# Kernel tuning notes

Hardware: AMD Instinct MI355X
Metric: run time of the kernel (lower is better)

The kernel has to match this reference:

```python
import jax, jax.numpy as jnp
import numpy as np

EMBED = 256
HID = EMBED * 4
NUM_EXPERTS = 4
WINDOW = 16
B, T = 4, 4096
EPS = 1e-5


def _ln(x, g, b):
    m = jnp.mean(x, axis=-1, keepdims=True)
    v = jnp.mean(jnp.square(x - m), axis=-1, keepdims=True)
    return (x - m) / jnp.sqrt(v + EPS) * g + b


def setup_inputs() -> dict:
    key = jax.random.key(0)
    ks = jax.random.split(key, 16)
    s = 0.02
    d = {
        'x': jax.random.normal(ks[0], (B, T, EMBED), jnp.float32),
        'ln1_g': jnp.ones((EMBED,), jnp.float32),
        'ln1_b': jnp.zeros((EMBED,), jnp.float32),
        'qkv_w': jax.random.normal(ks[1], (EMBED, 3 * EMBED), jnp.float32) * s,
        'qkv_b': jnp.zeros((3 * EMBED,), jnp.float32),
        'proj_w': jax.random.normal(ks[2], (EMBED, EMBED), jnp.float32) * s,
        'proj_b': jnp.zeros((EMBED,), jnp.float32),
        'attn_gate': jnp.ones((EMBED,), jnp.float32),
        'ln2_g': jnp.ones((EMBED,), jnp.float32),
        'ln2_b': jnp.zeros((EMBED,), jnp.float32),
        'gating_w': jax.random.normal(ks[3], (EMBED, NUM_EXPERTS), jnp.float32) * s,
        'gating_b': jnp.zeros((NUM_EXPERTS,), jnp.float32),
        'e_w1': jax.random.normal(ks[4], (NUM_EXPERTS, EMBED, HID), jnp.float32) * s,
        'e_b1': jnp.zeros((NUM_EXPERTS, HID), jnp.float32),
        'e_w2': jax.random.normal(ks[5], (NUM_EXPERTS, HID, EMBED), jnp.float32) * s,
        'e_b2': jnp.zeros((NUM_EXPERTS, EMBED), jnp.float32),
    }
    return d


def reference(x, ln1_g, ln1_b, qkv_w, qkv_b, proj_w, proj_b, attn_gate,
              ln2_g, ln2_b, gating_w, gating_b, e_w1, e_b1, e_w2, e_b2):
    Bx, Tx, C = x.shape
    # --- sparse attention branch ---
    h = _ln(x, ln1_g, ln1_b)
    qkv = h @ qkv_w + qkv_b                      # [B,T,3C]
    q, k, v = jnp.split(qkv, 3, axis=-1)
    scores = jnp.einsum('btc,bsc->bts', q, k) / jnp.sqrt(jnp.float32(C))
    idx = jnp.arange(Tx)
    diff = idx[:, None] - idx[None, :]           # i - j
    in_window = (diff >= 0) & (diff <= WINDOW)
    # faithful to torch code: scores outside the window (but causal) stay 0,
    # positions above the diagonal become -inf; softmax over full row
    scores = jnp.where(in_window, scores, 0.0)
    scores = jnp.where(diff >= 0, scores, -jnp.inf)
    att = jax.nn.softmax(scores, axis=-1)        # [B,T,T]
    a_out = jnp.einsum('bts,bsc->btc', att, v) * attn_gate
    x = x + a_out @ proj_w + proj_b
    # --- dense all-expert MoE branch ---
    h2 = _ln(x, ln2_g, ln2_b)
    gates = jax.nn.softmax(h2 @ gating_w + gating_b, axis=-1)     # [B,T,E]
    hid = jax.nn.gelu(jnp.einsum('btc,ech->bteh', h2, e_w1) + e_b1,
                      approximate=False)                           # [B,T,E,H]
    eo = jnp.einsum('bteh,eho->bteo', hid, e_w2) + e_b2            # [B,T,E,C]
    moe_out = jnp.einsum('bte,bteo->bto', gates, eo)
    return x + moe_out
```

## Files before the change

kernel.cpp:

```cpp
#include <hip/hip_runtime.h>
#include <hip/hip_bf16.h>
#include <math.h>

#define T_   4096
#define B_   4
#define C_   256
#define C3_  768
#define H_   1024
#define E_   4
#define M_   (B_*T_)
#define NCH_ 64
#define CHL_ (T_/NCH_)
#define KH_  4096

typedef __attribute__((ext_vector_type(8))) short short8;
typedef __attribute__((ext_vector_type(4))) float floatx4;

__device__ __forceinline__ float b2f(unsigned short u) {
  union { unsigned int i; float f; } x; x.i = ((unsigned int)u) << 16; return x.f;
}
__device__ __forceinline__ unsigned short f2b(float f) {
  __hip_bfloat16 h = __float2bfloat16(f);
  return *reinterpret_cast<unsigned short*>(&h);
}
__device__ __forceinline__ void unpack8(uint4 a, float* f) {
  unsigned int w[4] = {a.x, a.y, a.z, a.w};
  #pragma unroll
  for (int i = 0; i < 4; i++) {
    union { unsigned int u; float g; } lo, hi;
    lo.u = w[i] << 16; hi.u = w[i] & 0xffff0000u;
    f[2*i] = lo.g; f[2*i+1] = hi.g;
  }
}
__device__ __forceinline__ void gl_lds16(const void* g, void* l) {
  __builtin_amdgcn_global_load_lds(
      (const __attribute__((address_space(1))) void*)g,
      (__attribute__((address_space(3))) void*)l, 16, 0, 0);
}
__device__ __forceinline__ float gelu_s(float v) {
  float e = __expf(-1.702f * v);
  return v * __builtin_amdgcn_rcpf(1.0f + e);
}
__device__ __forceinline__ unsigned int pk_fp8x4(float a, float b, float c, float d) {
  unsigned int v = 0;
  v = __builtin_amdgcn_cvt_pk_fp8_f32(a, b, v, false);
  v = __builtin_amdgcn_cvt_pk_fp8_f32(c, d, v, true);
  return v;
}
__device__ __forceinline__ unsigned char f2fp8(float v) {
  return (unsigned char)(__builtin_amdgcn_cvt_pk_fp8_f32(v, v, 0, false) & 0xff);
}

__global__ __launch_bounds__(256) void transpose_cvt(
    const float* __restrict__ src, unsigned short* __restrict__ dst, int K, int N,
    int dstLd, size_t dstZStride) {
  __shared__ float tile[32][33];
  src += (size_t)blockIdx.z * K * N;
  dst += (size_t)blockIdx.z * dstZStride;
  int n0 = blockIdx.x * 32, k0 = blockIdx.y * 32;
  int tx = threadIdx.x, ty = threadIdx.y;
  #pragma unroll
  for (int i = 0; i < 32; i += 8)
    tile[ty + i][tx] = src[(size_t)(k0 + ty + i) * N + n0 + tx];
  __syncthreads();
  #pragma unroll
  for (int i = 0; i < 32; i += 8)
    dst[(size_t)(n0 + ty + i) * dstLd + k0 + tx] = f2b(tile[tx][ty + i]);
}

__global__ __launch_bounds__(256) void transpose_w2_fp8(
    const float* __restrict__ src, unsigned char* __restrict__ dst) {
  __shared__ float tile[32][33];
  int e = blockIdx.z;
  src += (size_t)e * H_ * C_;
  int h0 = blockIdx.x * 32, c0 = blockIdx.y * 32;
  int tx = threadIdx.x, ty = threadIdx.y;
  #pragma unroll
  for (int i = 0; i < 32; i += 8)
    tile[ty + i][tx] = src[(size_t)(h0 + ty + i) * C_ + c0 + tx];
  __syncthreads();
  int k = e * H_ + h0 + tx;
  int kp = (k & ~63) | ((k & 48) >> 2) | ((k & 12) << 2) | (k & 3);
  #pragma unroll
  for (int i = 0; i < 32; i += 8)
    dst[(size_t)(c0 + ty + i) * KH_ + kp] = f2fp8(tile[tx][ty + i] * 256.0f);
}

__global__ __launch_bounds__(256) void ln1_kernel(
    const float* __restrict__ x, const float* __restrict__ g,
    const float* __restrict__ b, unsigned short* __restrict__ h) {
  __shared__ float red[4];
  int row = blockIdx.x, tid = threadIdx.x;
  float v = x[(size_t)row * C_ + tid];
  float s = v;
  #pragma unroll
  for (int o = 32; o; o >>= 1) s += __shfl_xor(s, o);
  if ((tid & 63) == 0) red[tid >> 6] = s;
  __syncthreads();
  float mean = (red[0] + red[1] + red[2] + red[3]) * (1.0f / C_);
  __syncthreads();
  float d = v - mean;
  float q = d * d;
  #pragma unroll
  for (int o = 32; o; o >>= 1) q += __shfl_xor(q, o);
  if ((tid & 63) == 0) red[tid >> 6] = q;
  __syncthreads();
  float var = (red[0] + red[1] + red[2] + red[3]) * (1.0f / C_);
  h[(size_t)row * C_ + tid] = f2b(d * rsqrtf(var + 1e-5f) * g[tid] + b[tid]);
}

__global__ __launch_bounds__(256) void ln2_gates_kernel(
    const float* __restrict__ x1, const float* __restrict__ g,
    const float* __restrict__ b, const float* __restrict__ gw,
    const float* __restrict__ gb, unsigned short* __restrict__ h2,
    float* __restrict__ gates) {
  __shared__ float red[4];
  __shared__ float redg[4][4];
  int row = blockIdx.x, tid = threadIdx.x;
  float v = x1[(size_t)row * C_ + tid];
  float s = v;
  #pragma unroll
  for (int o = 32; o; o >>= 1) s += __shfl_xor(s, o);
  if ((tid & 63) == 0) red[tid >> 6] = s;
  __syncthreads();
  float mean = (red[0] + red[1] + red[2] + red[3]) * (1.0f / C_);
  __syncthreads();
  float d = v - mean;
  float q = d * d;
  #pragma unroll
  for (int o = 32; o; o >>= 1) q += __shfl_xor(q, o);
  if ((tid & 63) == 0) red[tid >> 6] = q;
  __syncthreads();
  float var = (red[0] + red[1] + red[2] + red[3]) * (1.0f / C_);
  float hv = d * rsqrtf(var + 1e-5f) * g[tid] + b[tid];
  h2[(size_t)row * C_ + tid] = f2b(hv);
  float p0 = hv * gw[tid * 4 + 0];
  float p1 = hv * gw[tid * 4 + 1];
  float p2 = hv * gw[tid * 4 + 2];
  float p3 = hv * gw[tid * 4 + 3];
  #pragma unroll
  for (int o = 32; o; o >>= 1) {
    p0 += __shfl_xor(p0, o); p1 += __shfl_xor(p1, o);
    p2 += __shfl_xor(p2, o); p3 += __shfl_xor(p3, o);
  }
  if ((tid & 63) == 0) {
    int w = tid >> 6;
    redg[w][0] = p0; redg[w][1] = p1; redg[w][2] = p2; redg[w][3] = p3;
  }
  __syncthreads();
  if (tid == 0) {
    float t4[4];
    #pragma unroll
    for (int e = 0; e < 4; e++)
      t4[e] = redg[0][e] + redg[1][e] + redg[2][e] + redg[3][e] + gb[e];
    float m = fmaxf(fmaxf(t4[0], t4[1]), fmaxf(t4[2], t4[3]));
    float zs = 0.f;
    #pragma unroll
    for (int e = 0; e < 4; e++) { t4[e] = __expf(t4[e] - m); zs += t4[e]; }
    float inv = 1.0f / zs;
    #pragma unroll
    for (int e = 0; e < 4; e++) gates[(size_t)row * 4 + e] = t4[e] * inv;
  }
}

__global__ __launch_bounds__(256) void scan1_kernel(const unsigned short* __restrict__ qkv,
                                                    float* __restrict__ S) {
  int b = blockIdx.x >> 6, ch = blockIdx.x & 63, c = threadIdx.x;
  float s = 0.f;
  size_t base = ((size_t)b * T_ + (size_t)ch * CHL_) * C3_ + 512 + c;
  for (int t = 0; t < CHL_; t++) s += b2f(qkv[base + (size_t)t * C3_]);
  S[((size_t)b * NCH_ + ch) * C_ + c] = s;
}
__global__ __launch_bounds__(256) void scan2_kernel(float* __restrict__ S) {
  int b = blockIdx.x, c = threadIdx.x;
  float run = 0.f;
  for (int ch = 0; ch < NCH_; ch++) {
    size_t i = ((size_t)b * NCH_ + ch) * C_ + c;
    float t = S[i]; S[i] = run; run += t;
  }
}
__global__ __launch_bounds__(256) void scan3_kernel(const unsigned short* __restrict__ qkv,
                                                    const float* __restrict__ S,
                                                    unsigned short* __restrict__ Pb) {
  int b = blockIdx.x >> 6, ch = blockIdx.x & 63, c = threadIdx.x;
  float run = S[((size_t)b * NCH_ + ch) * C_ + c];
  size_t row0 = (size_t)b * T_ + (size_t)ch * CHL_;
  for (int t = 0; t < CHL_; t++) {
    run += b2f(qkv[(row0 + t) * C3_ + 512 + c]);
    Pb[(row0 + t) * C_ + c] = f2b(run);
  }
}

__global__ __launch_bounds__(256) void attn_kernel(
    const unsigned short* __restrict__ qkv, const unsigned short* __restrict__ Pb,
    const float* __restrict__ gate, unsigned short* __restrict__ aout) {
  int wave = threadIdx.x >> 6, lane = threadIdx.x & 63;
  int r = blockIdx.x * 4 + wave;
  int t = r & (T_ - 1);
  int g = lane >> 4, u = lane & 15;
  const unsigned short* qp = qkv + (size_t)r * C3_ + (u << 4);
  float qv[16];
  unpack8(*(const uint4*)qp, qv);
  unpack8(*(const uint4*)(qp + 8), qv + 8);
  float sc[5];
  #pragma unroll
  for (int rnd = 0; rnd < 5; rnd++) {
    int j = rnd * 4 + g;
    int jj = t - 16 + j;
    bool valid = (j <= 16) && (jj >= 0);
    float d = 0.f;
    if (valid) {
      const unsigned short* kp = qkv + (size_t)(r - 16 + j) * C3_ + 256 + (u << 4);
      float kv[16];
      unpack8(*(const uint4*)kp, kv);
      unpack8(*(const uint4*)(kp + 8), kv + 8);
      #pragma unroll
      for (int c = 0; c < 16; c++) d += qv[c] * kv[c];
    }
    d += __shfl_xor(d, 1); d += __shfl_xor(d, 2);
    d += __shfl_xor(d, 4); d += __shfl_xor(d, 8);
    sc[rnd] = valid ? d * 0.0625f : -1e30f;
  }
  float m = fmaxf(fmaxf(fmaxf(sc[0], sc[1]), fmaxf(sc[2], sc[3])), sc[4]);
  m = fmaxf(m, __shfl_xor(m, 16));
  m = fmaxf(m, __shfl_xor(m, 32));
  if (t > 16) m = fmaxf(m, 0.0f);
  float ev[5], Zp = 0.f;
  #pragma unroll
  for (int rnd = 0; rnd < 5; rnd++) {
    ev[rnd] = (sc[rnd] > -1e29f) ? __expf(sc[rnd] - m) : 0.f;
    Zp += ev[rnd];
  }
  Zp += __shfl_xor(Zp, 16);
  Zp += __shfl_xor(Zp, 32);
  float e0v = 0.f;
  if (t > 16) { e0v = __expf(-m); Zp += e0v * (float)(t - 16); }
  float vp[16];
  #pragma unroll
  for (int c = 0; c < 16; c++) vp[c] = 0.f;
  #pragma unroll
  for (int rnd = 0; rnd < 5; rnd++) {
    if (ev[rnd] != 0.f) {
      int j = rnd * 4 + g;
      const unsigned short* vpp = qkv + (size_t)(r - 16 + j) * C3_ + 512 + (u << 4);
      float vv[16];
      unpack8(*(const uint4*)vpp, vv);
      unpack8(*(const uint4*)(vpp + 8), vv + 8);
      #pragma unroll
      for (int c = 0; c < 16; c++) vp[c] += ev[rnd] * vv[c];
    }
  }
  #pragma unroll
  for (int c = 0; c < 16; c++) {
    vp[c] += __shfl_xor(vp[c], 16);
    vp[c] += __shfl_xor(vp[c], 32);
  }
  if (g == 0) {
    if (t > 16) {
      const unsigned short* pp = Pb + (size_t)(r - 17) * C_ + (u << 4);
      float pv[16];
      unpack8(*(const uint4*)pp, pv);
      unpack8(*(const uint4*)(pp + 8), pv + 8);
      #pragma unroll
      for (int c = 0; c < 16; c++) vp[c] += e0v * pv[c];
    }
    float inv = 1.0f / Zp;
    const float* gp = gate + (u << 4);
    unsigned int ow[8];
    #pragma unroll
    for (int i = 0; i < 8; i++) {
      unsigned short lo = f2b(vp[2*i] * inv * gp[2*i]);
      unsigned short hi = f2b(vp[2*i+1] * inv * gp[2*i+1]);
      ow[i] = (unsigned int)lo | ((unsigned int)hi << 16);
    }
    uint4 s0 = {ow[0], ow[1], ow[2], ow[3]};
    uint4 s1 = {ow[4], ow[5], ow[6], ow[7]};
    *(uint4*)(aout + (size_t)r * C_ + (u << 4)) = s0;
    *(uint4*)(aout + (size_t)r * C_ + (u << 4) + 8) = s1;
  }
}

template<int EPI>
__global__ __launch_bounds__(256) void gemm128(
    const unsigned short* __restrict__ A, const unsigned short* __restrict__ Bt,
    const float* __restrict__ bias, int K, int ldOut,
    const float* __restrict__ resid, float* __restrict__ outf,
    unsigned short* __restrict__ outb, unsigned char* __restrict__ outf8,
    const float* __restrict__ gates) {
  __shared__ __align__(16) unsigned short As[128 * 64];
  __shared__ __align__(16) unsigned short Bs[128 * 64];
  const int tid = threadIdx.x;
  const int wave = tid >> 6, lane = tid & 63;
  const int mBlk = blockIdx.x * 128, nBlk = blockIdx.y * 128;
  const int wm = (wave >> 1) * 64, wn = (wave & 1) * 64;
  const int lm = lane & 15, lk = (lane >> 4) * 8;
  floatx4 acc[4][4];
  #pragma unroll
  for (int i = 0; i < 4; i++)
    #pragma unroll
    for (int j = 0; j < 4; j++) acc[i][j] = (floatx4){0.f, 0.f, 0.f, 0.f};

  for (int kt = 0; kt < K; kt += 64) {
    __syncthreads();
    #pragma unroll
    for (int i = 0; i < 4; i++) {
      int seg = i * 256 + tid;
      int row = seg >> 3, g = seg & 7;
      int gc = (g ^ (row & 7)) << 3;
      gl_lds16(A + (size_t)(mBlk + row) * K + kt + gc, &As[seg * 8]);
      gl_lds16(Bt + (size_t)(nBlk + row) * K + kt + gc, &Bs[seg * 8]);
    }
    __syncthreads();
    #pragma unroll
    for (int kk = 0; kk < 64; kk += 32) {
      short8 mf[4], nf[4];
      #pragma unroll
      for (int j = 0; j < 4; j++) {
        int row = wm + j * 16 + lm;
        mf[j] = *(const short8*)&As[row * 64 + ((((kk + lk) >> 3) ^ (row & 7)) << 3)];
      }
      #pragma unroll
      for (int i = 0; i < 4; i++) {
        int row = wn + i * 16 + lm;
        nf[i] = *(const short8*)&Bs[row * 64 + ((((kk + lk) >> 3) ^ (row & 7)) << 3)];
      }
      #pragma unroll
      for (int i = 0; i < 4; i++)
        #pragma unroll
        for (int j = 0; j < 4; j++)
          acc[i][j] = __builtin_amdgcn_mfma_f32_16x16x32_bf16(nf[i], mf[j], acc[i][j], 0, 0, 0);
    }
  }
  const int lc = lane & 15, quad = lane >> 4, q4 = quad * 4;
  if (EPI == 2) {
    const int eIdx = nBlk >> 10;
    #pragma unroll
    for (int j = 0; j < 4; j++) {
      int m = mBlk + wm + j * 16 + lc;
      float gs = 64.0f * gates[(size_t)m * E_ + eIdx];
      unsigned int w[4];
      #pragma unroll
      for (int i = 0; i < 4; i++) {
        int n0 = nBlk + wn + i * 16 + q4;
        float4 bs = *(const float4*)&bias[n0];
        w[i] = pk_fp8x4(gs * gelu_s(acc[i][j][0] + bs.x),
                        gs * gelu_s(acc[i][j][1] + bs.y),
                        gs * gelu_s(acc[i][j][2] + bs.z),
                        gs * gelu_s(acc[i][j][3] + bs.w));
      }
      uint4 st = {w[0], w[1], w[2], w[3]};
      *(uint4*)&outf8[(size_t)m * KH_ + nBlk + wn + quad * 16] = st;
    }
  } else {
    #pragma unroll
    for (int i = 0; i < 4; i++) {
      int n0 = nBlk + wn + i * 16 + q4;
      float4 bs = *(const float4*)&bias[n0];
      #pragma unroll
      for (int j = 0; j < 4; j++) {
        int m = mBlk + wm + j * 16 + lc;
        float v0 = acc[i][j][0] + bs.x, v1 = acc[i][j][1] + bs.y;
        float v2 = acc[i][j][2] + bs.z, v3 = acc[i][j][3] + bs.w;
        if (EPI == 0) {
          ushort4 o = {f2b(v0), f2b(v1), f2b(v2), f2b(v3)};
          *(ushort4*)&outb[(size_t)m * ldOut + n0] = o;
        } else {
          size_t idx = (size_t)m * ldOut + n0;
          float4 r = *(const float4*)&resid[idx];
          float4 o = {v0 + r.x, v1 + r.y, v2 + r.z, v3 + r.w};
          *(float4*)&outf[idx] = o;
        }
      }
    }
  }
}

__global__ __launch_bounds__(256) void gemm_down(
    const unsigned char* __restrict__ hid8, const unsigned char* __restrict__ w2f8,
    const float* __restrict__ b2, const float* __restrict__ gates,
    const float* __restrict__ x1, float* __restrict__ out) {
  __shared__ __align__(16) unsigned char As[128 * 128];
  __shared__ __align__(16) unsigned char Bs[64 * 128];
  const int tid = threadIdx.x;
  const int wave = tid >> 6, lane = tid & 63;
  const int mBlk = blockIdx.x * 128, nBlk = blockIdx.y * 64;
  const int wm = wave * 32;
  const int lm = lane & 15, quad = lane >> 4;
  floatx4 acc[4][2];
  #pragma unroll
  for (int i = 0; i < 4; i++)
    #pragma unroll
    for (int j = 0; j < 2; j++) acc[i][j] = (floatx4){0.f, 0.f, 0.f, 0.f};

  for (int kt = 0; kt < KH_; kt += 128) {
    __syncthreads();
    #pragma unroll
    for (int r = 0; r < 4; r++) {
      int seg = r * 256 + tid;
      int row = seg >> 3, s = seg & 7;
      int sp = s ^ (row & 7);
      gl_lds16(hid8 + (size_t)(mBlk + row) * KH_ + kt + sp * 16, &As[seg * 16]);
    }
    #pragma unroll
    for (int r = 0; r < 2; r++) {
      int seg = r * 256 + tid;
      int row = seg >> 3, s = seg & 7;
      int sp = s ^ (row & 7);
      gl_lds16(w2f8 + (size_t)(nBlk + row) * KH_ + kt + sp * 16, &Bs[seg * 16]);
    }
    __syncthreads();
    #pragma unroll
    for (int kk = 0; kk < 4; kk++) {
      int c8 = kk * 4 + quad;
      int s = c8 >> 1, h8 = (c8 & 1) * 8;
      long mf[2], nf[4];
      #pragma unroll
      for (int j = 0; j < 2; j++) {
        int row = wm + j * 16 + lm;
        mf[j] = *(const long*)&As[row * 128 + ((s ^ (row & 7)) << 4) + h8];
      }
      #pragma unroll
      for (int i = 0; i < 4; i++) {
        int row = i * 16 + lm;
        nf[i] = *(const long*)&Bs[row * 128 + ((s ^ (row & 7)) << 4) + h8];
      }
      #pragma unroll
      for (int i = 0; i < 4; i++)
        #pragma unroll
        for (int j = 0; j < 2; j++)
          acc[i][j] = __builtin_amdgcn_mfma_f32_16x16x32_fp8_fp8(nf[i], mf[j], acc[i][j], 0, 0, 0);
    }
  }
  const float sc = 1.0f / 16384.0f;
  const int q4 = quad * 4;
  #pragma unroll
  for (int j = 0; j < 2; j++) {
    int m = mBlk + wm + j * 16 + lm;
    float4 g4 = *(const float4*)(gates + (size_t)m * 4);
    #pragma unroll
    for (int i = 0; i < 4; i++) {
      int n0 = nBlk + i * 16 + q4;
      float4 bA = *(const float4*)&b2[0 * C_ + n0];
      float4 bB = *(const float4*)&b2[1 * C_ + n0];
      float4 bC = *(const float4*)&b2[2 * C_ + n0];
      float4 bD = *(const float4*)&b2[3 * C_ + n0];
      size_t idx = (size_t)m * C_ + n0;
      float4 r = *(const float4*)&x1[idx];
      float4 o;
      o.x = acc[i][j][0]*sc + r.x + g4.x*bA.x + g4.y*bB.x + g4.z*bC.x + g4.w*bD.x;
      o.y = acc[i][j][1]*sc + r.y + g4.x*bA.y + g4.y*bB.y + g4.z*bC.y + g4.w*bD.y;
      o.z = acc[i][j][2]*sc + r.z + g4.x*bA.z + g4.y*bB.z + g4.z*bC.z + g4.w*bD.z;
      o.w = acc[i][j][3]*sc + r.w + g4.x*bA.w + g4.y*bB.w + g4.z*bC.w + g4.w*bD.w;
      *(float4*)&out[idx] = o;
    }
  }
}

extern "C" void kernel_launch(void* const* d_in, const int* in_sizes, int n_in,
                              void* d_out, int out_size, void* d_ws, size_t ws_size,
                              hipStream_t stream) {
  const float* x       = (const float*)d_in[0];
  const float* ln1_g   = (const float*)d_in[1];
  const float* ln1_b   = (const float*)d_in[2];
  const float* qkv_w   = (const float*)d_in[3];
  const float* qkv_b   = (const float*)d_in[4];
  const float* proj_w  = (const float*)d_in[5];
  const float* proj_b  = (const float*)d_in[6];
  const float* attn_g  = (const float*)d_in[7];
  const float* ln2_g   = (const float*)d_in[8];
  const float* ln2_b   = (const float*)d_in[9];
  const float* gat_w   = (const float*)d_in[10];
  const float* gat_b   = (const float*)d_in[11];
  const float* e_w1    = (const float*)d_in[12];
  const float* e_b1    = (const float*)d_in[13];
  const float* e_w2    = (const float*)d_in[14];
  const float* e_b2    = (const float*)d_in[15];
  float* out = (float*)d_out;

  char* p = (char*)d_ws;
  unsigned short* h    = (unsigned short*)p; p += (size_t)M_ * C_ * 2;
  unsigned short* qkv  = (unsigned short*)p; p += (size_t)M_ * C3_ * 2;
  unsigned short* Pb   = (unsigned short*)p; p += (size_t)M_ * C_ * 2;
  unsigned short* aout = (unsigned short*)p; p += (size_t)M_ * C_ * 2;
  float*          x1   = (float*)p;          p += (size_t)M_ * C_ * 4;
  unsigned short* h2   = (unsigned short*)p; p += (size_t)M_ * C_ * 2;
  float*          gts  = (float*)p;          p += (size_t)M_ * E_ * 4;
  float*          S    = (float*)p;          p += (size_t)B_ * NCH_ * C_ * 4;
  unsigned short* wq   = (unsigned short*)p; p += (size_t)C3_ * C_ * 2;
  unsigned short* wp   = (unsigned short*)p; p += (size_t)C_ * C_ * 2;
  unsigned short* w1t  = (unsigned short*)p; p += (size_t)KH_ * C_ * 2;
  unsigned char*  w2f8 = (unsigned char*)p;  p += (size_t)C_ * KH_;
  unsigned char*  hid8 = (unsigned char*)p;  p += (size_t)M_ * KH_;

  dim3 t32x8(32, 8);
  transpose_cvt<<<dim3(C3_/32, C_/32, 1), t32x8, 0, stream>>>(qkv_w, wq, C_, C3_, C_, 0);
  transpose_cvt<<<dim3(C_/32, C_/32, 1),  t32x8, 0, stream>>>(proj_w, wp, C_, C_, C_, 0);
  transpose_cvt<<<dim3(H_/32, C_/32, E_), t32x8, 0, stream>>>(e_w1, w1t, C_, H_, C_, (size_t)H_ * C_);
  transpose_w2_fp8<<<dim3(H_/32, C_/32, E_), t32x8, 0, stream>>>(e_w2, w2f8);

  ln1_kernel<<<M_, 256, 0, stream>>>(x, ln1_g, ln1_b, h);
  gemm128<0><<<dim3(M_/128, C3_/128), 256, 0, stream>>>(h, wq, qkv_b, C_, C3_,
      nullptr, nullptr, qkv, nullptr, nullptr);
  scan1_kernel<<<B_*NCH_, 256, 0, stream>>>(qkv, S);
  scan2_kernel<<<B_, 256, 0, stream>>>(S);
  scan3_kernel<<<B_*NCH_, 256, 0, stream>>>(qkv, S, Pb);
  attn_kernel<<<M_/4, 256, 0, stream>>>(qkv, Pb, attn_g, aout);
  gemm128<1><<<dim3(M_/128, C_/128), 256, 0, stream>>>(aout, wp, proj_b, C_, C_,
      x, x1, nullptr, nullptr, nullptr);
  ln2_gates_kernel<<<M_, 256, 0, stream>>>(x1, ln2_g, ln2_b, gat_w, gat_b, h2, gts);
  gemm128<2><<<dim3(M_/128, KH_/128), 256, 0, stream>>>(h2, w1t, e_b1, C_, 0,
      nullptr, nullptr, nullptr, hid8, gts);
  gemm_down<<<dim3(M_/128, C_/64), 256, 0, stream>>>(hid8, w2f8, e_b2, gts, x1, out);
}
```

Before: 329.9 us.

## Fuse MoE up and down projections into one kernel keeping hidden in LDS

The two MoE kernels (the up-GEMM writing fp8 hidden activations to global memory, and the down-GEMM reading them back) are replaced by one kernel. Each block takes 64 rows and loops over 64-wide hidden chunks. W1 and W2 chunks are double-buffered in LDS, and the gelu'd, gated fp8 hidden tile stays in LDS before feeding the down MFMA. W2's fp8 layout is changed to a chunk-major swizzled form to match. This removes the 64 MB hidden round trip to HBM. The cost is only 256 blocks at one block per CU (launch_bounds 256,1, large LDS), more barriers per chunk, and recomputation of nothing.

```diff
diff --git a/kernel.cpp b/kernel.cpp
--- a/kernel.cpp
+++ b/kernel.cpp
@@ -50,6 +50,13 @@
 __device__ __forceinline__ unsigned char f2fp8(float v) {
   return (unsigned char)(__builtin_amdgcn_cvt_pk_fp8_f32(v, v, 0, false) & 0xff);
 }
+__device__ __forceinline__ float sel4(float4 v, int e) {
+  float r = v.x;
+  r = (e == 1) ? v.y : r;
+  r = (e == 2) ? v.z : r;
+  r = (e == 3) ? v.w : r;
+  return r;
+}
 
 __global__ __launch_bounds__(256) void transpose_cvt(
     const float* __restrict__ src, unsigned short* __restrict__ dst, int K, int N,
@@ -80,10 +87,13 @@
     tile[ty + i][tx] = src[(size_t)(h0 + ty + i) * C_ + c0 + tx];
   __syncthreads();
   int k = e * H_ + h0 + tx;
-  int kp = (k & ~63) | ((k & 48) >> 2) | ((k & 12) << 2) | (k & 3);
-  #pragma unroll
-  for (int i = 0; i < 32; i += 8)
-    dst[(size_t)(c0 + ty + i) * KH_ + kp] = f2fp8(tile[tx][ty + i] * 256.0f);
+  int chunk = k >> 6, kc = k & 63;
+  #pragma unroll
+  for (int i = 0; i < 32; i += 8) {
+    int c = c0 + ty + i;
+    int sw = ((((kc >> 4) ^ (c & 3)) << 4) | (kc & 15));
+    dst[((size_t)chunk * 256 + c) * 64 + sw] = f2fp8(tile[tx][ty + i] * 256.0f);
+  }
 }
 
 __global__ __launch_bounds__(256) void ln1_kernel(
@@ -285,8 +295,7 @@
     const unsigned short* __restrict__ A, const unsigned short* __restrict__ Bt,
     const float* __restrict__ bias, int K, int ldOut,
     const float* __restrict__ resid, float* __restrict__ outf,
-    unsigned short* __restrict__ outb, unsigned char* __restrict__ outf8,
-    const float* __restrict__ gates) {
+    unsigned short* __restrict__ outb) {
   __shared__ __align__(16) unsigned short As[128 * 64];
   __shared__ __align__(16) unsigned short Bs[128 * 64];
   const int tid = threadIdx.x;
@@ -332,114 +341,183 @@
     }
   }
   const int lc = lane & 15, quad = lane >> 4, q4 = quad * 4;
-  if (EPI == 2) {
-    const int eIdx = nBlk >> 10;
+  #pragma unroll
+  for (int i = 0; i < 4; i++) {
+    int n0 = nBlk + wn + i * 16 + q4;
+    float4 bs = *(const float4*)&bias[n0];
     #pragma unroll
     for (int j = 0; j < 4; j++) {
       int m = mBlk + wm + j * 16 + lc;
-      float gs = 64.0f * gates[(size_t)m * E_ + eIdx];
-      unsigned int w[4];
-      #pragma unroll
-      for (int i = 0; i < 4; i++) {
-        int n0 = nBlk + wn + i * 16 + q4;
-        float4 bs = *(const float4*)&bias[n0];
-        w[i] = pk_fp8x4(gs * gelu_s(acc[i][j][0] + bs.x),
-                        gs * gelu_s(acc[i][j][1] + bs.y),
-                        gs * gelu_s(acc[i][j][2] + bs.z),
-                        gs * gelu_s(acc[i][j][3] + bs.w));
-      }
-      uint4 st = {w[0], w[1], w[2], w[3]};
-      *(uint4*)&outf8[(size_t)m * KH_ + nBlk + wn + quad * 16] = st;
-    }
-  } else {
-    #pragma unroll
-    for (int i = 0; i < 4; i++) {
-      int n0 = nBlk + wn + i * 16 + q4;
-      float4 bs = *(const float4*)&bias[n0];
-      #pragma unroll
-      for (int j = 0; j < 4; j++) {
-        int m = mBlk + wm + j * 16 + lc;
-        float v0 = acc[i][j][0] + bs.x, v1 = acc[i][j][1] + bs.y;
-        float v2 = acc[i][j][2] + bs.z, v3 = acc[i][j][3] + bs.w;
-        if (EPI == 0) {
-          ushort4 o = {f2b(v0), f2b(v1), f2b(v2), f2b(v3)};
-          *(ushort4*)&outb[(size_t)m * ldOut + n0] = o;
-        } else {
-          size_t idx = (size_t)m * ldOut + n0;
-          float4 r = *(const float4*)&resid[idx];
-          float4 o = {v0 + r.x, v1 + r.y, v2 + r.z, v3 + r.w};
-          *(float4*)&outf[idx] = o;
-        }
-      }
-    }
-  }
-}
-
-__global__ __launch_bounds__(256) void gemm_down(
-    const unsigned char* __restrict__ hid8, const unsigned char* __restrict__ w2f8,
-    const float* __restrict__ b2, const float* __restrict__ gates,
-    const float* __restrict__ x1, float* __restrict__ out) {
-  __shared__ __align__(16) unsigned char As[128 * 128];
-  __shared__ __align__(16) unsigned char Bs[64 * 128];
+      float v0 = acc[i][j][0] + bs.x, v1 = acc[i][j][1] + bs.y;
+      float v2 = acc[i][j][2] + bs.z, v3 = acc[i][j][3] + bs.w;
+      if (EPI == 0) {
+        ushort4 o = {f2b(v0), f2b(v1), f2b(v2), f2b(v3)};
+        *(ushort4*)&outb[(size_t)m * ldOut + n0] = o;
+      } else {
+        size_t idx = (size_t)m * ldOut + n0;
+        float4 r = *(const float4*)&resid[idx];
+        float4 o = {v0 + r.x, v1 + r.y, v2 + r.z, v3 + r.w};
+        *(float4*)&outf[idx] = o;
+      }
+    }
+  }
+}
+
+__global__ __launch_bounds__(256, 1) void moe_fused(
+    const unsigned short* __restrict__ h2,
+    const unsigned short* __restrict__ w1t,
+    const float* __restrict__ b1,
+    const unsigned char* __restrict__ w2b,
+    const float* __restrict__ b2,
+    const float* __restrict__ gates,
+    const float* __restrict__ x1,
+    float* __restrict__ out) {
+  __shared__ __align__(16) unsigned short As[64 * 256];
+  __shared__ __align__(16) unsigned short W1s[2][64 * 256];
+  __shared__ __align__(16) unsigned char  W2s[2][256 * 64];
+  __shared__ __align__(16) unsigned char  Hs[64 * 64];
+  __shared__ __align__(16) float          B1s[2][64];
   const int tid = threadIdx.x;
   const int wave = tid >> 6, lane = tid & 63;
-  const int mBlk = blockIdx.x * 128, nBlk = blockIdx.y * 64;
-  const int wm = wave * 32;
   const int lm = lane & 15, quad = lane >> 4;
-  floatx4 acc[4][2];
+  const int mb = blockIdx.x * 64;
+  const int wmu = (wave >> 1) * 32;
+  const int whu = (wave & 1) * 32;
+  const int wc  = wave * 64;
+
+  #pragma unroll
+  for (int t = 0; t < 8; t++) {
+    int seg = t * 256 + tid;
+    int row = seg >> 5, g = seg & 31;
+    int gp = (g & 24) | ((g & 7) ^ (row & 7));
+    gl_lds16(h2 + (size_t)(mb + row) * C_ + gp * 8, &As[seg * 8]);
+  }
+
+  auto stageW = [&](int c, int buf) {
+    const unsigned short* ws = w1t + (size_t)c * 64 * C_;
+    #pragma unroll
+    for (int t = 0; t < 8; t++) {
+      int seg = t * 256 + tid;
+      int row = seg >> 5, g = seg & 31;
+      int gp = (g & 24) | ((g & 7) ^ (row & 7));
+      gl_lds16(ws + (size_t)row * C_ + gp * 8, &W1s[buf][seg * 8]);
+    }
+    const unsigned char* vs = w2b + (size_t)c * 256 * 64;
+    #pragma unroll
+    for (int t = 0; t < 4; t++) {
+      int seg = t * 256 + tid;
+      gl_lds16(vs + (size_t)seg * 16, &W2s[buf][seg * 16]);
+    }
+    if (lane < 16)
+      gl_lds16(b1 + (size_t)c * 64 + lane * 4, &B1s[buf][0]);
+  };
+
+  stageW(0, 0);
+
+  float4 ga[2];
+  #pragma unroll
+  for (int j = 0; j < 2; j++)
+    ga[j] = *(const float4*)(gates + (size_t)(mb + wmu + j * 16 + lm) * 4);
+
+  floatx4 dacc[4][4];
   #pragma unroll
   for (int i = 0; i < 4; i++)
     #pragma unroll
-    for (int j = 0; j < 2; j++) acc[i][j] = (floatx4){0.f, 0.f, 0.f, 0.f};
-
-  for (int kt = 0; kt < KH_; kt += 128) {
-    __syncthreads();
-    #pragma unroll
-    for (int r = 0; r < 4; r++) {
-      int seg = r * 256 + tid;
-      int row = seg >> 3, s = seg & 7;
-      int sp = s ^ (row & 7);
-      gl_lds16(hid8 + (size_t)(mBlk + row) * KH_ + kt + sp * 16, &As[seg * 16]);
-    }
-    #pragma unroll
-    for (int r = 0; r < 2; r++) {
-      int seg = r * 256 + tid;
-      int row = seg >> 3, s = seg & 7;
-      int sp = s ^ (row & 7);
-      gl_lds16(w2f8 + (size_t)(nBlk + row) * KH_ + kt + sp * 16, &Bs[seg * 16]);
-    }
-    __syncthreads();
-    #pragma unroll
-    for (int kk = 0; kk < 4; kk++) {
-      int c8 = kk * 4 + quad;
-      int s = c8 >> 1, h8 = (c8 & 1) * 8;
-      long mf[2], nf[4];
+    for (int j = 0; j < 4; j++) dacc[i][j] = (floatx4){0.f, 0.f, 0.f, 0.f};
+
+  asm volatile("s_waitcnt vmcnt(0)" ::: "memory");
+  __builtin_amdgcn_s_barrier();
+  __builtin_amdgcn_sched_barrier(0);
+
+  for (int c = 0; c < 64; c++) {
+    const int cb = c & 1;
+    __builtin_amdgcn_s_barrier();
+    __builtin_amdgcn_sched_barrier(0);
+    stageW((c + 1) & 63, cb ^ 1);
+    asm volatile("s_waitcnt vmcnt(13)" ::: "memory");
+    __builtin_amdgcn_s_barrier();
+    __builtin_amdgcn_sched_barrier(0);
+
+    floatx4 uacc[2][2];
+    #pragma unroll
+    for (int i = 0; i < 2; i++)
+      #pragma unroll
+      for (int j = 0; j < 2; j++) uacc[i][j] = (floatx4){0.f, 0.f, 0.f, 0.f};
+    #pragma unroll
+    for (int kk = 0; kk < 8; kk++) {
+      int kc = kk * 4 + quad;
+      short8 mf[2], nf[2];
       #pragma unroll
       for (int j = 0; j < 2; j++) {
-        int row = wm + j * 16 + lm;
-        mf[j] = *(const long*)&As[row * 128 + ((s ^ (row & 7)) << 4) + h8];
+        int row = wmu + j * 16 + lm;
+        mf[j] = *(const short8*)&As[row * 256 + ((kc ^ (row & 7)) << 3)];
+      }
+      #pragma unroll
+      for (int i = 0; i < 2; i++) {
+        int row = whu + i * 16 + lm;
+        nf[i] = *(const short8*)&W1s[cb][row * 256 + ((kc ^ (row & 7)) << 3)];
+      }
+      #pragma unroll
+      for (int i = 0; i < 2; i++)
+        #pragma unroll
+        for (int j = 0; j < 2; j++)
+          uacc[i][j] = __builtin_amdgcn_mfma_f32_16x16x32_bf16(nf[i], mf[j], uacc[i][j], 0, 0, 0);
+    }
+
+    int e = c >> 4;
+    float gs0 = 64.0f * sel4(ga[0], e);
+    float gs1 = 64.0f * sel4(ga[1], e);
+    #pragma unroll
+    for (int i = 0; i < 2; i++) {
+      float4 bb = *(const float4*)&B1s[cb][whu + i * 16 + quad * 4];
+      #pragma unroll
+      for (int j = 0; j < 2; j++) {
+        float gs = j ? gs1 : gs0;
+        unsigned int w = pk_fp8x4(gs * gelu_s(uacc[i][j][0] + bb.x),
+                                  gs * gelu_s(uacc[i][j][1] + bb.y),
+                                  gs * gelu_s(uacc[i][j][2] + bb.z),
+                                  gs * gelu_s(uacc[i][j][3] + bb.w));
+        int m = wmu + j * 16 + lm;
+        int hh = whu + i * 16 + quad * 4;
+        *(unsigned int*)&Hs[m * 64 + ((((hh >> 3) ^ (m & 7)) << 3) | (hh & 7))] = w;
+      }
+    }
+    asm volatile("s_waitcnt lgkmcnt(0)" ::: "memory");
+    __builtin_amdgcn_s_barrier();
+    __builtin_amdgcn_sched_barrier(0);
+
+    #pragma unroll
+    for (int kk = 0; kk < 2; kk++) {
+      long mfh[4], nfw[4];
+      #pragma unroll
+      for (int j = 0; j < 4; j++) {
+        int m = j * 16 + lm;
+        int g8 = quad + 4 * kk;
+        mfh[j] = *(const long*)&Hs[m * 64 + ((g8 ^ (m & 7)) << 3)];
       }
       #pragma unroll
       for (int i = 0; i < 4; i++) {
-        int row = i * 16 + lm;
-        nf[i] = *(const long*)&Bs[row * 128 + ((s ^ (row & 7)) << 4) + h8];
+        int cr = wc + i * 16 + lm;
+        int sl = ((quad >> 1) + 2 * kk) ^ (cr & 3);
+        nfw[i] = *(const long*)&W2s[cb][cr * 64 + (sl << 4) + ((quad & 1) << 3)];
       }
       #pragma unroll
       for (int i = 0; i < 4; i++)
         #pragma unroll
-        for (int j = 0; j < 2; j++)
-          acc[i][j] = __builtin_amdgcn_mfma_f32_16x16x32_fp8_fp8(nf[i], mf[j], acc[i][j], 0, 0, 0);
-    }
-  }
+        for (int j = 0; j < 4; j++)
+          dacc[i][j] = __builtin_amdgcn_mfma_f32_16x16x32_fp8_fp8(nfw[i], mfh[j], dacc[i][j], 0, 0, 0);
+    }
+  }
+
   const float sc = 1.0f / 16384.0f;
   const int q4 = quad * 4;
   #pragma unroll
-  for (int j = 0; j < 2; j++) {
-    int m = mBlk + wm + j * 16 + lm;
+  for (int j = 0; j < 4; j++) {
+    int m = mb + j * 16 + lm;
     float4 g4 = *(const float4*)(gates + (size_t)m * 4);
     #pragma unroll
     for (int i = 0; i < 4; i++) {
-      int n0 = nBlk + i * 16 + q4;
+      int n0 = wc + i * 16 + q4;
       float4 bA = *(const float4*)&b2[0 * C_ + n0];
       float4 bB = *(const float4*)&b2[1 * C_ + n0];
       float4 bC = *(const float4*)&b2[2 * C_ + n0];
@@ -447,10 +525,10 @@
       size_t idx = (size_t)m * C_ + n0;
       float4 r = *(const float4*)&x1[idx];
       float4 o;
-      o.x = acc[i][j][0]*sc + r.x + g4.x*bA.x + g4.y*bB.x + g4.z*bC.x + g4.w*bD.x;
-      o.y = acc[i][j][1]*sc + r.y + g4.x*bA.y + g4.y*bB.y + g4.z*bC.y + g4.w*bD.y;
-      o.z = acc[i][j][2]*sc + r.z + g4.x*bA.z + g4.y*bB.z + g4.z*bC.z + g4.w*bD.z;
-      o.w = acc[i][j][3]*sc + r.w + g4.x*bA.w + g4.y*bB.w + g4.z*bC.w + g4.w*bD.w;
+      o.x = dacc[i][j][0]*sc + r.x + g4.x*bA.x + g4.y*bB.x + g4.z*bC.x + g4.w*bD.x;
+      o.y = dacc[i][j][1]*sc + r.y + g4.x*bA.y + g4.y*bB.y + g4.z*bC.y + g4.w*bD.y;
+      o.z = dacc[i][j][2]*sc + r.z + g4.x*bA.z + g4.y*bB.z + g4.z*bC.z + g4.w*bD.z;
+      o.w = dacc[i][j][3]*sc + r.w + g4.x*bA.w + g4.y*bB.w + g4.z*bC.w + g4.w*bD.w;
       *(float4*)&out[idx] = o;
     }
   }
@@ -490,7 +568,6 @@
   unsigned short* wp   = (unsigned short*)p; p += (size_t)C_ * C_ * 2;
   unsigned short* w1t  = (unsigned short*)p; p += (size_t)KH_ * C_ * 2;
   unsigned char*  w2f8 = (unsigned char*)p;  p += (size_t)C_ * KH_;
-  unsigned char*  hid8 = (unsigned char*)p;  p += (size_t)M_ * KH_;
 
   dim3 t32x8(32, 8);
   transpose_cvt<<<dim3(C3_/32, C_/32, 1), t32x8, 0, stream>>>(qkv_w, wq, C_, C3_, C_, 0);
@@ -500,15 +577,13 @@
 
   ln1_kernel<<<M_, 256, 0, stream>>>(x, ln1_g, ln1_b, h);
   gemm128<0><<<dim3(M_/128, C3_/128), 256, 0, stream>>>(h, wq, qkv_b, C_, C3_,
-      nullptr, nullptr, qkv, nullptr, nullptr);
+      nullptr, nullptr, qkv);
   scan1_kernel<<<B_*NCH_, 256, 0, stream>>>(qkv, S);
   scan2_kernel<<<B_, 256, 0, stream>>>(S);
   scan3_kernel<<<B_*NCH_, 256, 0, stream>>>(qkv, S, Pb);
   attn_kernel<<<M_/4, 256, 0, stream>>>(qkv, Pb, attn_g, aout);
   gemm128<1><<<dim3(M_/128, C_/128), 256, 0, stream>>>(aout, wp, proj_b, C_, C_,
-      x, x1, nullptr, nullptr, nullptr);
+      x, x1, nullptr);
   ln2_gates_kernel<<<M_, 256, 0, stream>>>(x1, ln2_g, ln2_b, gat_w, gat_b, h2, gts);
-  gemm128<2><<<dim3(M_/128, KH_/128), 256, 0, stream>>>(h2, w1t, e_b1, C_, 0,
-      nullptr, nullptr, nullptr, hid8, gts);
-  gemm_down<<<dim3(M_/128, C_/64), 256, 0, stream>>>(hid8, w2f8, e_b2, gts, x1, out);
-}
+  moe_fused<<<M_/64, 256, 0, stream>>>(h2, w1t, e_b1, w2f8, e_b2, gts, x1, out);
+}
```

Result: slower. 348.4 us (+5.6%).
